# Optimization experiments

Measured on AMD Instinct MI355X. Metric: run time of the kernel, lower is better.

Reference implementation:

```python
import jax, jax.numpy as jnp
import numpy as np

UNITS = 128
FILTERS = 32
KSIZE = 31
B, T, DV, DQ = 64, 1000, 512, 1024


def setup_inputs() -> dict:
    key = jax.random.key(0)
    ks = jax.random.split(key, 12)
    scale = 0.05
    inp = {
        "query": jax.random.normal(ks[0], (B, DQ), jnp.float32),
        "values": jax.random.normal(ks[1], (B, T, DV), jnp.float32),
        "previous_attention_weights": jax.random.uniform(ks[2], (B, T, 1), jnp.float32),
        # learned params
        "Wq": jax.random.normal(ks[3], (DQ, UNITS), jnp.float32) * scale,
        "bq": jnp.zeros((UNITS,), jnp.float32),
        "Wm": jax.random.normal(ks[4], (DV, UNITS), jnp.float32) * scale,
        "bm": jnp.zeros((UNITS,), jnp.float32),
        "Wv": jax.random.normal(ks[5], (UNITS, 1), jnp.float32) * scale,
        "bv": jnp.zeros((1,), jnp.float32),
        "Wconv": jax.random.normal(ks[6], (KSIZE, 1, FILTERS), jnp.float32) * scale,  # [W, Cin, Cout]
        "Wl": jax.random.normal(ks[7], (FILTERS, UNITS), jnp.float32) * scale,
    }
    return inp


def _forward(query, values, prev_w, Wq, bq, Wm, bm, Wv, bv, Wconv, Wl):
    # location features: Conv1D (same padding, no bias) then Dense(tanh, no bias)
    loc = jax.lax.conv_general_dilated(
        prev_w, Wconv, window_strides=(1,), padding="SAME",
        dimension_numbers=("NWC", "WIO", "NWC"))          # [B, T, FILTERS]
    loc = jnp.tanh(loc @ Wl)                                # [B, T, UNITS]
    q = query @ Wq + bq                                     # [B, UNITS]
    m = values @ Wm + bm                                    # [B, T, UNITS]
    score = jnp.tanh(m + q[:, None, :] + loc) @ Wv + bv     # [B, T, 1]
    attention_weights = jax.nn.softmax(score, axis=1)       # softmax over time
    context = jnp.sum(attention_weights * values, axis=1)   # [B, DV]
    return context, attention_weights


def reference(query, values, previous_attention_weights, Wq, bq, Wm, bm, Wv, bv, Wconv, Wl):
    return _forward(query, values, previous_attention_weights,
                    Wq, bq, Wm, bm, Wv, bv, Wconv, Wl)
```

## Files before the change

kernel.cpp:

```cpp
#include <hip/hip_runtime.h>

#define B_  64
#define T_  1000
#define DV_ 512
#define DQ_ 1024
#define U_  128
#define F_  32
#define KS_ 31
#define P_  16
#define CT_ 63

typedef __attribute__((ext_vector_type(8))) short short8;
typedef __attribute__((ext_vector_type(4))) float f32x4;

__device__ __forceinline__ unsigned pk2(float a, float b) {
    union { float f; unsigned u; } x, y;
    x.f = a; y.f = b;
    unsigned ra = (x.u + 0x7FFFu + ((x.u >> 16) & 1u)) >> 16;
    unsigned rb = (y.u + 0x7FFFu + ((y.u >> 16) & 1u)) >> 16;
    return (ra & 0xFFFFu) | (rb << 16);
}

__device__ __forceinline__ float fast_tanh(float x) {
    return 1.0f - 2.0f / (__expf(2.0f * x) + 1.0f);
}

__device__ __forceinline__ short8 pk8(float4 f0, float4 f1) {
    int4 q;
    q.x = pk2(f0.x, f0.y); q.y = pk2(f0.z, f0.w);
    q.z = pk2(f1.x, f1.y); q.w = pk2(f1.z, f1.w);
    return *(short8*)&q;
}

__device__ __forceinline__ void gload_lds16(const void* g, void* l) {
    __builtin_amdgcn_global_load_lds(
        (const __attribute__((address_space(1))) unsigned*)g,
        (__attribute__((address_space(3))) unsigned*)l, 16, 0, 0);
}

__global__ __launch_bounds__(1024) void prep_qb_kernel(
    const float* __restrict__ Wm, const float* __restrict__ Wl,
    const float* __restrict__ query, const float* __restrict__ Wq,
    const float* __restrict__ bq, const float* __restrict__ bm,
    short* __restrict__ WmX, short* __restrict__ WlX, float* __restrict__ qb)
{
    __shared__ float sh[DQ_ + 8 * U_];
    int blk = blockIdx.x, tid = threadIdx.x;
    if (blk < 9) {
        int g = blk * 1024 + tid;
        if (g < 8192) {
            int kc = g >> 9, e = g & 511;
            int n = e >> 2, q = e & 3;
            int kb = kc * 32 + q * 8;
            int4 p;
            p.x = pk2(Wm[(kb + 0) * U_ + n], Wm[(kb + 1) * U_ + n]);
            p.y = pk2(Wm[(kb + 2) * U_ + n], Wm[(kb + 3) * U_ + n]);
            p.z = pk2(Wm[(kb + 4) * U_ + n], Wm[(kb + 5) * U_ + n]);
            p.w = pk2(Wm[(kb + 6) * U_ + n], Wm[(kb + 7) * U_ + n]);
            ((int4*)WmX)[g] = p;
        } else if (g < 8704) {
            int e = g - 8192;
            int n = e >> 2, q = e & 3;
            int kb = q * 8;
            int4 p;
            p.x = pk2(Wl[(kb + 0) * U_ + n], Wl[(kb + 1) * U_ + n]);
            p.y = pk2(Wl[(kb + 2) * U_ + n], Wl[(kb + 3) * U_ + n]);
            p.z = pk2(Wl[(kb + 4) * U_ + n], Wl[(kb + 5) * U_ + n]);
            p.w = pk2(Wl[(kb + 6) * U_ + n], Wl[(kb + 7) * U_ + n]);
            ((int4*)WlX)[e] = p;
        }
    } else {
        float* qs = sh;
        float* red = sh + DQ_;
        int b = blk - 9;
        qs[tid] = query[b * DQ_ + tid];
        __syncthreads();
        int u = tid & 127, p = tid >> 7;
        float a = 0.f;
        const float* wp = Wq + (size_t)p * 128 * U_ + u;
        const float* qp = qs + p * 128;
#pragma unroll 8
        for (int k = 0; k < 128; ++k) a += qp[k] * wp[(size_t)k * U_];
        red[p * U_ + u] = a;
        __syncthreads();
        if (tid < U_) {
            float s = bq[tid] + bm[tid];
#pragma unroll
            for (int pp = 0; pp < 8; ++pp) s += red[pp * U_ + tid];
            qb[b * U_ + tid] = s;
        }
    }
}

__global__ __launch_bounds__(256, 3) void score_kernel(
    const float* __restrict__ values, const float* __restrict__ prev,
    const float* __restrict__ Wc, const float* __restrict__ Wv,
    const float* __restrict__ bv, const short* __restrict__ WmX,
    const short* __restrict__ WlX, const float* __restrict__ qb,
    float* __restrict__ scores)
{
    __shared__ float As[2][64 * 64];
    __shared__ short AsL[64 * 32];
    __shared__ float WcS[KS_ * F_];
    __shared__ float qbS[2 * U_];
    __shared__ float WvS[U_];

    const int tid = threadIdx.x;
    const int r0 = blockIdx.x * 64;
    const int b0 = r0 / T_;
    const int b1 = (r0 + 63) / T_;

    const int wv = tid >> 6, lane = tid & 63;
    const int quad = lane >> 4, m15 = lane & 15;
    const int esw = (m15 & 3) << 1;
    const int lrow = lane >> 4;
    const int lunit = (lane & 15) ^ (lrow << 1);

    const int4* bW  = (const int4*)WmX + m15 * 4 + quad;
    const int4* blW = (const int4*)WlX + m15 * 4 + quad;

    auto stage = [&](int buf, int k0) {
#pragma unroll
        for (int j = 0; j < 4; ++j) {
            const float* src = values + (size_t)(r0 + wv * 16 + j * 4 + lrow) * DV_
                               + k0 + lunit * 4;
            gload_lds16(src, &As[buf][(wv * 16 + j * 4) * 64]);
        }
    };

    stage(0, 0);
    int4 bfA[8], bfB[8];
#pragma unroll
    for (int c = 0; c < 8; ++c) bfA[c] = bW[c * 64];

    for (int i = tid; i < KS_ * F_; i += 256) WcS[i] = Wc[i];
    if (tid < U_) WvS[tid] = Wv[tid];
    {
        int bb = (tid < U_) ? b0 : b1;
        qbS[tid] = qb[bb * U_ + (tid & (U_ - 1))];
    }
    __syncthreads();

    {
        int i = tid & 63, fg = tid >> 6;
        int r = r0 + i;
        int b = r / T_;
        int t = r - b * T_;
        const float* pv = prev + b * T_;
        float a8[8] = {};
#pragma unroll
        for (int k = 0; k < KS_; ++k) {
            int tt = t + k - 15;
            float p = ((unsigned)tt < (unsigned)T_) ? pv[tt] : 0.f;
#pragma unroll
            for (int j = 0; j < 8; ++j) a8[j] += p * WcS[k * F_ + fg * 8 + j];
        }
        int4 pq;
        pq.x = pk2(a8[0], a8[1]); pq.y = pk2(a8[2], a8[3]);
        pq.z = pk2(a8[4], a8[5]); pq.w = pk2(a8[6], a8[7]);
        ((int4*)AsL)[i * 4 + (fg ^ ((i >> 1) & 3))] = pq;
    }
    __syncthreads();

    const int row = wv * 16 + m15;
    f32x4 acc[8] = {};
    {
        short8 afl = ((const short8*)AsL)[row * 4 + (quad ^ ((row >> 1) & 3))];
#pragma unroll
        for (int c = 0; c < 8; ++c) {
            int4 bl = blW[c * 64];
            acc[c] = __builtin_amdgcn_mfma_f32_16x16x32_bf16(afl, *(short8*)&bl, acc[c], 0, 0, 0);
        }
        int qoff[4];
#pragma unroll
        for (int v = 0; v < 4; ++v) {
            int r = r0 + wv * 16 + quad * 4 + v;
            qoff[v] = ((r / T_) == b0) ? 0 : U_;
        }
#pragma unroll
        for (int c = 0; c < 8; ++c) {
            int col = c * 16 + m15;
#pragma unroll
            for (int v = 0; v < 4; ++v)
                acc[c][v] = qbS[qoff[v] + col] + fast_tanh(acc[c][v]);
        }
    }
    __syncthreads();

#pragma unroll
    for (int s = 0; s < 8; ++s) {
        if (s + 1 < 8) stage((s + 1) & 1, (s + 1) * 64);
#pragma unroll
        for (int c = 0; c < 8; ++c) bfB[c] = bW[(2 * s + 1) * 512 + c * 64];

        const float4* ap = (const float4*)&As[s & 1][row * 64];
        {
            int u0 = (2 * quad) ^ esw;
            float4 f0 = ap[u0], f1 = ap[u0 + 1];
            short8 af = pk8(f0, f1);
#pragma unroll
            for (int c = 0; c < 8; ++c)
                acc[c] = __builtin_amdgcn_mfma_f32_16x16x32_bf16(af, *(short8*)&bfB[0] == *(short8*)&bfB[0] ? *(short8*)&bfA[c] : *(short8*)&bfA[c], acc[c], 0, 0, 0);
        }
        int4 bfN[8];
        if (s + 1 < 8) {
#pragma unroll
            for (int c = 0; c < 8; ++c) bfN[c] = bW[(2 * s + 2) * 512 + c * 64];
        }
        {
            int u0 = (2 * (4 + quad)) ^ esw;
            float4 f0 = ap[u0], f1 = ap[u0 + 1];
            short8 af = pk8(f0, f1);
#pragma unroll
            for (int c = 0; c < 8; ++c)
                acc[c] = __builtin_amdgcn_mfma_f32_16x16x32_bf16(af, *(short8*)&bfB[c], acc[c], 0, 0, 0);
        }
#pragma unroll
        for (int c = 0; c < 8; ++c) bfA[c] = bfN[c];
        __syncthreads();
    }

    float psum[4] = {0.f, 0.f, 0.f, 0.f};
#pragma unroll
    for (int c = 0; c < 8; ++c) {
        int col = c * 16 + m15;
        float wvv = WvS[col];
#pragma unroll
        for (int v = 0; v < 4; ++v)
            psum[v] += fast_tanh(acc[c][v]) * wvv;
    }
#pragma unroll
    for (int off = 1; off < 16; off <<= 1) {
#pragma unroll
        for (int v = 0; v < 4; ++v) psum[v] += __shfl_xor(psum[v], off);
    }
    if (m15 == 0) {
        float bvv = bv[0];
#pragma unroll
        for (int v = 0; v < 4; ++v)
            scores[r0 + wv * 16 + quad * 4 + v] = psum[v] + bvv;
    }
}

__global__ __launch_bounds__(256) void ctxsm_kernel(
    const float* __restrict__ scores, const float* __restrict__ values,
    float* __restrict__ attw, float* __restrict__ part)
{
    __shared__ float sS[1024];
    __shared__ float red[4];
    __shared__ float4 ps[128];
    int b = blockIdx.x, p = blockIdx.y, tid = threadIdx.x;
    const float* sb = scores + b * T_;
    float v[4];
#pragma unroll
    for (int i = 0; i < 4; ++i) {
        int t = tid + i * 256;
        v[i] = (t < T_) ? sb[t] : -1e30f;
        sS[t] = v[i];
    }
    float mx = fmaxf(fmaxf(v[0], v[1]), fmaxf(v[2], v[3]));
#pragma unroll
    for (int off = 32; off >= 1; off >>= 1) mx = fmaxf(mx, __shfl_xor(mx, off));
    int wvi = tid >> 6, lane = tid & 63;
    if (lane == 0) red[wvi] = mx;
    __syncthreads();
    mx = fmaxf(fmaxf(red[0], red[1]), fmaxf(red[2], red[3]));
    float sum = 0.f;
#pragma unroll
    for (int i = 0; i < 4; ++i)
        sum += (tid + i * 256 < T_) ? __expf(v[i] - mx) : 0.f;
#pragma unroll
    for (int off = 32; off >= 1; off >>= 1) sum += __shfl_xor(sum, off);
    __syncthreads();
    if (lane == 0) red[wvi] = sum;
    __syncthreads();
    float inv = 1.0f / (red[0] + red[1] + red[2] + red[3]);

    int t0 = p * CT_;
    int len = (T_ - t0 < CT_) ? (T_ - t0) : CT_;
    if (tid < len) attw[b * T_ + t0 + tid] = __expf(sS[t0 + tid] - mx) * inv;

    int cl = tid & 127, tp = tid >> 7;
    const float* vp = values + ((size_t)b * T_ + t0) * DV_ + cl * 4;
    float4 a = {0.f, 0.f, 0.f, 0.f};
#pragma unroll 4
    for (int t = tp; t < len; t += 2) {
        float4 vv = *(const float4*)(vp + (size_t)t * DV_);
        float wt = __expf(sS[t0 + t] - mx) * inv;
        a.x += wt * vv.x; a.y += wt * vv.y; a.z += wt * vv.z; a.w += wt * vv.w;
    }
    if (tp == 1) ps[cl] = a;
    __syncthreads();
    if (tp == 0) {
        float4 o = ps[cl];
        o.x += a.x; o.y += a.y; o.z += a.z; o.w += a.w;
        *(float4*)(part + ((size_t)(b * P_ + p)) * DV_ + cl * 4) = o;
    }
}

__global__ void ctx2_kernel(const float* __restrict__ part, float* __restrict__ ctx) {
    int b = blockIdx.x, tid = threadIdx.x;
    const float* pp = part + (size_t)b * P_ * DV_ + tid * 4;
    float4 s = {0.f, 0.f, 0.f, 0.f};
#pragma unroll
    for (int p = 0; p < P_; ++p) {
        float4 v = *(const float4*)(pp + (size_t)p * DV_);
        s.x += v.x; s.y += v.y; s.z += v.z; s.w += v.w;
    }
    *(float4*)(ctx + (size_t)b * DV_ + tid * 4) = s;
}

extern "C" void kernel_launch(void* const* d_in, const int* in_sizes, int n_in,
                              void* d_out, int out_size, void* d_ws, size_t ws_size,
                              hipStream_t stream) {
    const float* query  = (const float*)d_in[0];
    const float* values = (const float*)d_in[1];
    const float* prev   = (const float*)d_in[2];
    const float* Wq     = (const float*)d_in[3];
    const float* bq     = (const float*)d_in[4];
    const float* Wm     = (const float*)d_in[5];
    const float* bm     = (const float*)d_in[6];
    const float* Wv     = (const float*)d_in[7];
    const float* bv     = (const float*)d_in[8];
    const float* Wc     = (const float*)d_in[9];
    const float* Wl     = (const float*)d_in[10];

    float* out  = (float*)d_out;
    float* ctx  = out;
    float* attw = out + B_ * DV_;

    char* ws = (char*)d_ws;
    float* qb     = (float*)(ws);
    float* scores = (float*)(ws + 32768);
    short* WmX    = (short*)(ws + 288768);
    short* WlX    = (short*)(ws + 419840);
    float* part   = (float*)(ws + 428032);

    prep_qb_kernel<<<73, 1024, 0, stream>>>(Wm, Wl, query, Wq, bq, bm, WmX, WlX, qb);
    score_kernel<<<1000, 256, 0, stream>>>(values, prev, Wc, Wv, bv, WmX, WlX, qb, scores);
    ctxsm_kernel<<<dim3(B_, P_), 256, 0, stream>>>(scores, values, attw, part);
    ctx2_kernel<<<B_, 128, 0, stream>>>(part, ctx);
}
```

Baseline: 323.8 us.

## Alias shared-memory buffers, drop weight prefetch registers, raise occupancy to four blocks

Shared memory is packed into one byte array in which the second staging buffer also holds the location-feature tile and conv weights, shrinking LDS per block. The launch bound goes from 3 to 4 blocks per CU, and the double-buffered register prefetch of Wm fragments is replaced by loads issued just before each MFMA group, cutting register pressure. The XOR swizzle of the staged values tile becomes a rotation swizzle. Latency hiding now depends on more resident waves rather than register prefetch, so Wm load latency may be exposed if occupancy does not actually rise.

```diff
diff --git a/kernel.cpp b/kernel.cpp
--- a/kernel.cpp
+++ b/kernel.cpp
@@ -92,18 +92,20 @@
     }
 }
 
-__global__ __launch_bounds__(256, 3) void score_kernel(
+__global__ __launch_bounds__(256, 4) void score_kernel(
     const float* __restrict__ values, const float* __restrict__ prev,
     const float* __restrict__ Wc, const float* __restrict__ Wv,
     const float* __restrict__ bv, const short* __restrict__ WmX,
     const short* __restrict__ WlX, const float* __restrict__ qb,
     float* __restrict__ scores)
 {
-    __shared__ float As[2][64 * 64];
-    __shared__ short AsL[64 * 32];
-    __shared__ float WcS[KS_ * F_];
-    __shared__ float qbS[2 * U_];
-    __shared__ float WvS[U_];
+    __shared__ char smem[2 * 16384 + 1024 + 512];
+    float* As0 = (float*)smem;
+    float* As1 = (float*)(smem + 16384);
+    short* AsL = (short*)(smem + 16384);
+    float* WcS = (float*)(smem + 16384 + 4096);
+    float* qbS = (float*)(smem + 32768);
+    float* WvS = (float*)(smem + 32768 + 1024);
 
     const int tid = threadIdx.x;
     const int r0 = blockIdx.x * 64;
@@ -112,26 +114,24 @@
 
     const int wv = tid >> 6, lane = tid & 63;
     const int quad = lane >> 4, m15 = lane & 15;
-    const int esw = (m15 & 3) << 1;
+    const int row = wv * 16 + m15;
     const int lrow = lane >> 4;
-    const int lunit = (lane & 15) ^ (lrow << 1);
 
     const int4* bW  = (const int4*)WmX + m15 * 4 + quad;
     const int4* blW = (const int4*)WlX + m15 * 4 + quad;
 
-    auto stage = [&](int buf, int k0) {
+    auto stage = [&](float* dst, int k0) {
 #pragma unroll
         for (int j = 0; j < 4; ++j) {
+            int R = ((j & 1) << 2) + lrow;
+            int lu = ((lane & 15) + R) & 15;
             const float* src = values + (size_t)(r0 + wv * 16 + j * 4 + lrow) * DV_
-                               + k0 + lunit * 4;
-            gload_lds16(src, &As[buf][(wv * 16 + j * 4) * 64]);
+                               + k0 + lu * 4;
+            gload_lds16(src, dst + (wv * 16 + j * 4) * 64);
         }
     };
 
-    stage(0, 0);
-    int4 bfA[8], bfB[8];
-#pragma unroll
-    for (int c = 0; c < 8; ++c) bfA[c] = bW[c * 64];
+    stage(As0, 0);
 
     for (int i = tid; i < KS_ * F_; i += 256) WcS[i] = Wc[i];
     if (tid < U_) WvS[tid] = Wv[tid];
@@ -162,7 +162,6 @@
     }
     __syncthreads();
 
-    const int row = wv * 16 + m15;
     f32x4 acc[8] = {};
     {
         short8 afl = ((const short8*)AsL)[row * 4 + (quad ^ ((row >> 1) & 3))];
@@ -187,36 +186,34 @@
     }
     __syncthreads();
 
+    const int Rr = m15 & 7;
 #pragma unroll
     for (int s = 0; s < 8; ++s) {
-        if (s + 1 < 8) stage((s + 1) & 1, (s + 1) * 64);
-#pragma unroll
-        for (int c = 0; c < 8; ++c) bfB[c] = bW[(2 * s + 1) * 512 + c * 64];
-
-        const float4* ap = (const float4*)&As[s & 1][row * 64];
+        if (s < 7) stage((s & 1) ? As0 : As1, (s + 1) * 64);
+        const float4* ap = (const float4*)(((s & 1) ? As1 : As0) + row * 64);
+        int4 bf[8];
+#pragma unroll
+        for (int c = 0; c < 8; ++c) bf[c] = bW[(2 * s) * 512 + c * 64];
         {
-            int u0 = (2 * quad) ^ esw;
-            float4 f0 = ap[u0], f1 = ap[u0 + 1];
+            int x = quad * 2;
+            float4 f0 = ap[(x - Rr) & 15];
+            float4 f1 = ap[(x + 1 - Rr) & 15];
             short8 af = pk8(f0, f1);
 #pragma unroll
             for (int c = 0; c < 8; ++c)
-                acc[c] = __builtin_amdgcn_mfma_f32_16x16x32_bf16(af, *(short8*)&bfB[0] == *(short8*)&bfB[0] ? *(short8*)&bfA[c] : *(short8*)&bfA[c], acc[c], 0, 0, 0);
-        }
-        int4 bfN[8];
-        if (s + 1 < 8) {
-#pragma unroll
-            for (int c = 0; c < 8; ++c) bfN[c] = bW[(2 * s + 2) * 512 + c * 64];
-        }
+                acc[c] = __builtin_amdgcn_mfma_f32_16x16x32_bf16(af, *(short8*)&bf[c], acc[c], 0, 0, 0);
+        }
+#pragma unroll
+        for (int c = 0; c < 8; ++c) bf[c] = bW[(2 * s + 1) * 512 + c * 64];
         {
-            int u0 = (2 * (4 + quad)) ^ esw;
-            float4 f0 = ap[u0], f1 = ap[u0 + 1];
+            int x = 8 + quad * 2;
+            float4 f0 = ap[(x - Rr) & 15];
+            float4 f1 = ap[(x + 1 - Rr) & 15];
             short8 af = pk8(f0, f1);
 #pragma unroll
             for (int c = 0; c < 8; ++c)
-                acc[c] = __builtin_amdgcn_mfma_f32_16x16x32_bf16(af, *(short8*)&bfB[c], acc[c], 0, 0, 0);
-        }
-#pragma unroll
-        for (int c = 0; c < 8; ++c) bfA[c] = bfN[c];
+                acc[c] = __builtin_amdgcn_mfma_f32_16x16x32_bf16(af, *(short8*)&bf[c], acc[c], 0, 0, 0);
+        }
         __syncthreads();
     }
 
```

Result: slower. 337.7 us (+4.3%).
